# Performance work log

Hardware: AMD Instinct MI355X
Metric: run time of the kernel (lower is better)

## Reference

```python
import jax, jax.numpy as jnp
import numpy as np

OUT, IN = 4096, 4096
NNZ = 838860  # 0.05 * OUT * IN
ALPHA = 1.0   # set_privacy(True)


def setup_inputs() -> dict:
    key = jax.random.key(0)
    k1, k2, k3, k4, k5, k6 = jax.random.split(key, 6)
    x = jax.random.normal(k1, (2, 2048, IN), dtype=jnp.float32)
    # packed uint4 pairs stored as bytes (kept in int32 per spec; values in [0,256))
    base_packed = jax.random.randint(k2, (OUT, IN // 2), 0, 256, dtype=jnp.int32)
    # per-row dequant scales (positive, small, like ceiling/7)
    scales = jax.random.uniform(k3, (OUT, 1), dtype=jnp.float32, minval=1e-3, maxval=5e-2)
    ortho_vals = jax.random.normal(k4, (NNZ,), dtype=jnp.float32) * 0.02
    ortho_rows = jax.random.randint(k5, (NNZ,), 0, OUT, dtype=jnp.int32)
    ortho_cols = jax.random.randint(k6, (NNZ,), 0, IN, dtype=jnp.int32)
    return {"x": x, "base_packed": base_packed, "scales": scales,
            "ortho_vals": ortho_vals, "ortho_rows": ortho_rows, "ortho_cols": ortho_cols}


def _dequant(base_packed, scales):
    # unpack two int4 values per byte: col 2k <- low nibble, col 2k+1 <- high nibble
    p = base_packed.astype(jnp.int32)
    low = p & 0xF
    high = (p >> 4) & 0xF
    O, K = p.shape
    w_int4 = jnp.stack([low, high], axis=-1).reshape(O, 2 * K) - 8  # offset-binary -> [-8, 7]
    return w_int4.astype(jnp.float32) * scales  # [O, I]


def reference(x, base_packed, scales, ortho_vals, ortho_rows, ortho_cols):
    O = base_packed.shape[0]
    I = 2 * base_packed.shape[1]
    w_base = _dequant(base_packed, scales)  # [O, I] fp32
    # sparse outlier residual scattered into dense weight (CSR spmm equivalent)
    w_corr = jnp.zeros((O, I), jnp.float32).at[ortho_rows, ortho_cols].add(ortho_vals)
    w = w_base + ALPHA * w_corr
    x_flat = x.reshape(-1, I).astype(jnp.float32)
    out = x_flat @ w.T  # [N, O]
    return out.reshape(x.shape[:-1] + (O,)).astype(x.dtype)
```

## Files before the change

kernel.cpp:

```cpp
#include <hip/hip_runtime.h>
#include <cstdint>
#include <cstddef>

typedef __bf16 bf16x8 __attribute__((ext_vector_type(8)));
typedef float f32x4 __attribute__((ext_vector_type(4)));
typedef unsigned short ushort8 __attribute__((ext_vector_type(8)));

#define OUT_DIM 4096
#define IN_DIM 4096
#define NT 64


__device__ __forceinline__ unsigned short f2bf(float f) {
  unsigned u = __float_as_uint(f);
  return (unsigned short)((u + 0x7FFFu + ((u >> 16) & 1u)) >> 16);
}

__device__ __forceinline__ void async_copy16(const void* g, void* l) {
  __builtin_amdgcn_global_load_lds(
      (const __attribute__((address_space(1))) unsigned int*)g,
      (__attribute__((address_space(3))) unsigned int*)l, 16, 0, 0);
}


__global__ __launch_bounds__(256) void scatter_kernel(
    const float* __restrict__ vals, const int* __restrict__ rows,
    const int* __restrict__ cols, float* __restrict__ delta, int nnz) {
  int i = blockIdx.x * 256 + threadIdx.x;
  if (i < nnz) {
    atomicAdd(&delta[(size_t)rows[i] * IN_DIM + cols[i]], vals[i]);
  }
}

__global__ __launch_bounds__(256) void dequant_fused_kernel(
    const int* __restrict__ packed, const float* __restrict__ scales,
    const float* __restrict__ delta, unsigned short* __restrict__ wb) {
  int idx = blockIdx.x * 256 + threadIdx.x;
  int4 p = reinterpret_cast<const int4*>(packed)[idx];
  float s = scales[idx >> 9];
  float4 d0 = reinterpret_cast<const float4*>(delta)[idx * 2];
  float4 d1 = reinterpret_cast<const float4*>(delta)[idx * 2 + 1];
  ushort8 o;
  o[0] = f2bf((float)((p.x & 15) - 8) * s + d0.x);
  o[1] = f2bf((float)(((p.x >> 4) & 15) - 8) * s + d0.y);
  o[2] = f2bf((float)((p.y & 15) - 8) * s + d0.z);
  o[3] = f2bf((float)(((p.y >> 4) & 15) - 8) * s + d0.w);
  o[4] = f2bf((float)((p.z & 15) - 8) * s + d1.x);
  o[5] = f2bf((float)(((p.z >> 4) & 15) - 8) * s + d1.y);
  o[6] = f2bf((float)((p.w & 15) - 8) * s + d1.z);
  o[7] = f2bf((float)(((p.w >> 4) & 15) - 8) * s + d1.w);
  *reinterpret_cast<ushort8*>(&wb[(size_t)idx * 8]) = o;
}

__global__ __launch_bounds__(256) void cvt_kernel(
    const float* __restrict__ in, unsigned short* __restrict__ out) {
  int i = blockIdx.x * 256 + threadIdx.x;
  float4 a = reinterpret_cast<const float4*>(in)[2 * i];
  float4 b = reinterpret_cast<const float4*>(in)[2 * i + 1];
  ushort8 o;
  o[0] = f2bf(a.x); o[1] = f2bf(a.y); o[2] = f2bf(a.z); o[3] = f2bf(a.w);
  o[4] = f2bf(b.x); o[5] = f2bf(b.y); o[6] = f2bf(b.z); o[7] = f2bf(b.w);
  *reinterpret_cast<ushort8*>(&out[(size_t)i * 8]) = o;
}


#define SLABOFF(buf, op, kh) ((((buf) * 4) + ((op) * 2) + (kh)) * 8192)

#define STAGE(buf, op, kh, kt)                                              \
  do {                                                                      \
    const unsigned short* g_ = ((op) ? gB : gA) + (kt) * 64 + (kh) * 32;    \
    unsigned short* l_ = (unsigned short*)lds + SLABOFF(buf, op, kh) + wave * 512; \
    async_copy16(g_, l_);                                                   \
    async_copy16(g_ + 128 * IN_DIM, l_ + 4096);                             \
  } while (0)

#define MFMA_ __builtin_amdgcn_mfma_f32_16x16x32_bf16

#define PHASE(BUF, KS, MH, READB, STAGEST, DOWAIT)                          \
  do {                                                                      \
    const unsigned short* as_ = (const unsigned short*)lds + SLABOFF(BUF, 0, KS); \
    bf16x8 a0_ = *(const bf16x8*)(as_ + offA[(MH) * 4 + 0]);                \
    bf16x8 a1_ = *(const bf16x8*)(as_ + offA[(MH) * 4 + 1]);                \
    bf16x8 a2_ = *(const bf16x8*)(as_ + offA[(MH) * 4 + 2]);                \
    bf16x8 a3_ = *(const bf16x8*)(as_ + offA[(MH) * 4 + 3]);                \
    if (READB) {                                                            \
      const unsigned short* bs_ = (const unsigned short*)lds + SLABOFF(BUF, 1, KS); \
      bB0 = *(const bf16x8*)(bs_ + offB[0]);                                \
      bB1 = *(const bf16x8*)(bs_ + offB[1]);                                \
      bB2 = *(const bf16x8*)(bs_ + offB[2]);                                \
      bB3 = *(const bf16x8*)(bs_ + offB[3]);                                \
    }                                                                       \
    STAGEST;                                                                \
    if (DOWAIT) asm volatile("s_waitcnt vmcnt(8)" ::: "memory");            \
    __builtin_amdgcn_s_barrier();                                           \
    asm volatile("s_waitcnt lgkmcnt(0)" ::: "memory");                      \
    __builtin_amdgcn_sched_barrier(0);                                      \
    __builtin_amdgcn_s_setprio(1);                                          \
    acc[(MH) * 4 + 0][0] = MFMA_(a0_, bB0, acc[(MH) * 4 + 0][0], 0, 0, 0);  \
    acc[(MH) * 4 + 0][1] = MFMA_(a0_, bB1, acc[(MH) * 4 + 0][1], 0, 0, 0);  \
    acc[(MH) * 4 + 0][2] = MFMA_(a0_, bB2, acc[(MH) * 4 + 0][2], 0, 0, 0);  \
    acc[(MH) * 4 + 0][3] = MFMA_(a0_, bB3, acc[(MH) * 4 + 0][3], 0, 0, 0);  \
    acc[(MH) * 4 + 1][0] = MFMA_(a1_, bB0, acc[(MH) * 4 + 1][0], 0, 0, 0);  \
    acc[(MH) * 4 + 1][1] = MFMA_(a1_, bB1, acc[(MH) * 4 + 1][1], 0, 0, 0);  \
    acc[(MH) * 4 + 1][2] = MFMA_(a1_, bB2, acc[(MH) * 4 + 1][2], 0, 0, 0);  \
    acc[(MH) * 4 + 1][3] = MFMA_(a1_, bB3, acc[(MH) * 4 + 1][3], 0, 0, 0);  \
    acc[(MH) * 4 + 2][0] = MFMA_(a2_, bB0, acc[(MH) * 4 + 2][0], 0, 0, 0);  \
    acc[(MH) * 4 + 2][1] = MFMA_(a2_, bB1, acc[(MH) * 4 + 2][1], 0, 0, 0);  \
    acc[(MH) * 4 + 2][2] = MFMA_(a2_, bB2, acc[(MH) * 4 + 2][2], 0, 0, 0);  \
    acc[(MH) * 4 + 2][3] = MFMA_(a2_, bB3, acc[(MH) * 4 + 2][3], 0, 0, 0);  \
    acc[(MH) * 4 + 3][0] = MFMA_(a3_, bB0, acc[(MH) * 4 + 3][0], 0, 0, 0);  \
    acc[(MH) * 4 + 3][1] = MFMA_(a3_, bB1, acc[(MH) * 4 + 3][1], 0, 0, 0);  \
    acc[(MH) * 4 + 3][2] = MFMA_(a3_, bB2, acc[(MH) * 4 + 3][2], 0, 0, 0);  \
    acc[(MH) * 4 + 3][3] = MFMA_(a3_, bB3, acc[(MH) * 4 + 3][3], 0, 0, 0);  \
    __builtin_amdgcn_s_setprio(0);                                          \
    __builtin_amdgcn_s_barrier();                                           \
  } while (0)

#define MINC(x) ((x) < NT ? (x) : (NT - 1))

#define TILE(BUF, t)                                                        \
  do {                                                                      \
    PHASE(BUF, 0, 0, true, STAGE(1 - (BUF), 0, 1, MINC((t) + 1)), false);   \
    PHASE(BUF, 0, 1, false, STAGE(1 - (BUF), 1, 1, MINC((t) + 1)), true);   \
    PHASE(BUF, 1, 0, true, STAGE(BUF, 0, 0, MINC((t) + 2)), false);         \
    PHASE(BUF, 1, 1, false, STAGE(BUF, 1, 0, MINC((t) + 2)), true);         \
  } while (0)

__global__ __launch_bounds__(512, 2) void gemm_kernel(
    const unsigned short* __restrict__ A,
    const unsigned short* __restrict__ B,
    float* __restrict__ C) {
  __shared__ __align__(16) unsigned short lds[65536];

  const int bid = blockIdx.x;
  const int xcd = bid & 7, i_ = bid >> 3;
  const int bm = (xcd >> 1) * 4 + (i_ >> 3);
  const int bn = (xcd & 1) * 8 + (i_ & 7);
  const int m0 = bm * 256, n0 = bn * 256;

  const int tid = threadIdx.x;
  const int wave = tid >> 6, lane = tid & 63;
  const int wm = wave >> 2, wn = wave & 3;
  const int lrow = lane & 15, lk = lane >> 4;

  const int r0 = tid >> 2, s0 = tid & 3;
  const int s0s = s0 ^ ((r0 >> 1) & 3);
  const unsigned short* gA = A + (size_t)(m0 + r0) * IN_DIM + s0s * 8;
  const unsigned short* gB = B + (size_t)(n0 + r0) * IN_DIM + s0s * 8;

  const int lks = lk ^ ((lrow >> 1) & 3);
  int offA[8], offB[4];
#pragma unroll
  for (int i = 0; i < 8; ++i) offA[i] = (wm * 128 + i * 16 + lrow) * 32 + lks * 8;
#pragma unroll
  for (int i = 0; i < 4; ++i) offB[i] = (wn * 64 + i * 16 + lrow) * 32 + lks * 8;

  f32x4 acc[8][4];
#pragma unroll
  for (int mi = 0; mi < 8; ++mi)
#pragma unroll
    for (int ni = 0; ni < 4; ++ni) acc[mi][ni] = (f32x4){0.f, 0.f, 0.f, 0.f};

  STAGE(0, 0, 0, 0); STAGE(0, 1, 0, 0);
  asm volatile("" ::: "memory");
  STAGE(0, 0, 1, 0); STAGE(0, 1, 1, 0);
  asm volatile("" ::: "memory");
  STAGE(1, 0, 0, 1); STAGE(1, 1, 0, 1);
  asm volatile("s_waitcnt vmcnt(8)" ::: "memory");
  __builtin_amdgcn_s_barrier();

  bf16x8 bB0, bB1, bB2, bB3;
#pragma unroll 1
  for (int p = 0; p < NT / 2; ++p) {
    const int te = 2 * p;
    TILE(0, te);
    TILE(1, te + 1);
  }
  asm volatile("s_waitcnt vmcnt(0)" ::: "memory");

#pragma unroll
  for (int mi = 0; mi < 8; ++mi)
#pragma unroll
    for (int ni = 0; ni < 4; ++ni) {
      int m = m0 + wm * 128 + mi * 16 + lk * 4;
      int n = n0 + wn * 64 + ni * 16 + lrow;
      float* cp = &C[(size_t)m * OUT_DIM + n];
#pragma unroll
      for (int r = 0; r < 4; ++r) cp[(size_t)r * OUT_DIM] = acc[mi][ni][r];
    }
}


extern "C" void kernel_launch(void* const* d_in, const int* in_sizes, int n_in,
                              void* d_out, int out_size, void* d_ws, size_t ws_size,
                              hipStream_t stream) {
  const float* x      = (const float*)d_in[0];
  const int*   packed = (const int*)d_in[1];
  const float* scales = (const float*)d_in[2];
  const float* vals   = (const float*)d_in[3];
  const int*   rows   = (const int*)d_in[4];
  const int*   cols   = (const int*)d_in[5];
  float* out = (float*)d_out;

  const int nnz = in_sizes[3];

  char* ws = (char*)d_ws;
  const size_t MB = 1024 * 1024;
  unsigned short* Wb = (unsigned short*)ws;
  unsigned short* Xb = (unsigned short*)(ws + 32 * MB);
  float*          Dl = (float*)(ws + 64 * MB);

  hipMemsetAsync(Dl, 0, 64 * MB, stream);
  scatter_kernel<<<(nnz + 255) / 256, 256, 0, stream>>>(vals, rows, cols, Dl, nnz);
  dequant_fused_kernel<<<8192, 256, 0, stream>>>(packed, scales, Dl, Wb);
  cvt_kernel<<<8192, 256, 0, stream>>>(x, Xb);
  gemm_kernel<<<256, 512, 0, stream>>>(Xb, Wb, out);
}
```

Baseline: 212.7 us.

## Scatter sparse outliers directly into bf16 weights via CAS, drop fp32 delta buffer

Removes the 64 MB fp32 delta buffer, its memset and the dequant kernel's reads of it. The kernel now dequantizes to bf16 first, then adds the sparse outlier values straight into the bf16 weights with a 32-bit atomicCAS loop on packed halfword pairs. This cuts roughly 192 MB of memory traffic. In exchange it adds CAS retry overhead and per-addition bf16 rounding, so duplicate indices are accumulated at bf16 precision instead of fp32.

```diff
diff --git a/kernel.cpp b/kernel.cpp
--- a/kernel.cpp
+++ b/kernel.cpp
@@ -23,33 +23,44 @@
 }
 
 
-__global__ __launch_bounds__(256) void scatter_kernel(
-    const float* __restrict__ vals, const int* __restrict__ rows,
-    const int* __restrict__ cols, float* __restrict__ delta, int nnz) {
-  int i = blockIdx.x * 256 + threadIdx.x;
-  if (i < nnz) {
-    atomicAdd(&delta[(size_t)rows[i] * IN_DIM + cols[i]], vals[i]);
-  }
-}
-
-__global__ __launch_bounds__(256) void dequant_fused_kernel(
+__global__ __launch_bounds__(256) void dequant_kernel(
     const int* __restrict__ packed, const float* __restrict__ scales,
-    const float* __restrict__ delta, unsigned short* __restrict__ wb) {
+    unsigned short* __restrict__ wb) {
   int idx = blockIdx.x * 256 + threadIdx.x;
   int4 p = reinterpret_cast<const int4*>(packed)[idx];
   float s = scales[idx >> 9];
-  float4 d0 = reinterpret_cast<const float4*>(delta)[idx * 2];
-  float4 d1 = reinterpret_cast<const float4*>(delta)[idx * 2 + 1];
   ushort8 o;
-  o[0] = f2bf((float)((p.x & 15) - 8) * s + d0.x);
-  o[1] = f2bf((float)(((p.x >> 4) & 15) - 8) * s + d0.y);
-  o[2] = f2bf((float)((p.y & 15) - 8) * s + d0.z);
-  o[3] = f2bf((float)(((p.y >> 4) & 15) - 8) * s + d0.w);
-  o[4] = f2bf((float)((p.z & 15) - 8) * s + d1.x);
-  o[5] = f2bf((float)(((p.z >> 4) & 15) - 8) * s + d1.y);
-  o[6] = f2bf((float)((p.w & 15) - 8) * s + d1.z);
-  o[7] = f2bf((float)(((p.w >> 4) & 15) - 8) * s + d1.w);
+  o[0] = f2bf((float)((p.x & 15) - 8) * s);
+  o[1] = f2bf((float)(((p.x >> 4) & 15) - 8) * s);
+  o[2] = f2bf((float)((p.y & 15) - 8) * s);
+  o[3] = f2bf((float)(((p.y >> 4) & 15) - 8) * s);
+  o[4] = f2bf((float)((p.z & 15) - 8) * s);
+  o[5] = f2bf((float)(((p.z >> 4) & 15) - 8) * s);
+  o[6] = f2bf((float)((p.w & 15) - 8) * s);
+  o[7] = f2bf((float)(((p.w >> 4) & 15) - 8) * s);
   *reinterpret_cast<ushort8*>(&wb[(size_t)idx * 8]) = o;
+}
+
+__global__ __launch_bounds__(256) void scatter_bf16_kernel(
+    const float* __restrict__ vals, const int* __restrict__ rows,
+    const int* __restrict__ cols, unsigned short* __restrict__ wb, int nnz) {
+  int i = blockIdx.x * 256 + threadIdx.x;
+  if (i >= nnz) return;
+  size_t idx = (size_t)rows[i] * IN_DIM + cols[i];
+  unsigned int* word = (unsigned int*)(wb + (idx & ~(size_t)1));
+  const bool hi = (idx & 1) != 0;
+  const float v = vals[i];
+  unsigned int old = *word, assumed;
+  do {
+    assumed = old;
+    unsigned short h = hi ? (unsigned short)(assumed >> 16)
+                          : (unsigned short)(assumed & 0xFFFFu);
+    float f = __uint_as_float((unsigned)h << 16);
+    unsigned short nh = f2bf(f + v);
+    unsigned int nw = hi ? ((assumed & 0x0000FFFFu) | ((unsigned)nh << 16))
+                         : ((assumed & 0xFFFF0000u) | (unsigned)nh);
+    old = atomicCAS(word, assumed, nw);
+  } while (old != assumed);
 }
 
 __global__ __launch_bounds__(256) void cvt_kernel(
@@ -208,11 +219,9 @@
   const size_t MB = 1024 * 1024;
   unsigned short* Wb = (unsigned short*)ws;
   unsigned short* Xb = (unsigned short*)(ws + 32 * MB);
-  float*          Dl = (float*)(ws + 64 * MB);
-
-  hipMemsetAsync(Dl, 0, 64 * MB, stream);
-  scatter_kernel<<<(nnz + 255) / 256, 256, 0, stream>>>(vals, rows, cols, Dl, nnz);
-  dequant_fused_kernel<<<8192, 256, 0, stream>>>(packed, scales, Dl, Wb);
+
+  dequant_kernel<<<8192, 256, 0, stream>>>(packed, scales, Wb);
+  scatter_bf16_kernel<<<(nnz + 255) / 256, 256, 0, stream>>>(vals, rows, cols, Wb, nnz);
   cvt_kernel<<<8192, 256, 0, stream>>>(x, Xb);
   gemm_kernel<<<256, 512, 0, stream>>>(Xb, Wb, out);
 }
```

Measured after the change: 187.8 us. 1.13x faster.
